# Optimization experiments

Measured on AMD Instinct MI355X. Metric: run time of the kernel, lower is better.

Reference implementation:

```python
import jax, jax.numpy as jnp
import numpy as np

N_NODES, N_EDGES = 1600, 32000
C = 128            # sphere_channels
LMAX, MMAX = 6, 2
M0 = LMAX + 1      # number of m=0 coefficients (7)
N_SPH = (LMAX + 1) ** 2   # 49 full harmonics after inverse Wigner rotation
BASIS = 512        # distance expansion size
MAX_ELEM = 90
HID = 128
RESCALE = 23.395238876342773


def _build_to_m(lmax, mmax):
    # CoefficientMappingModule.to_m: permutation from l-primary to m-primary order
    m_c = []
    for l in range(lmax + 1):
        mm = min(mmax, l)
        m_c.extend(range(-mm, mm + 1))
    m_c = np.array(m_c)
    n = len(m_c)
    to_m = np.zeros((n, n), np.float32)
    off = 0
    for m in range(mmax + 1):
        idx_r = np.nonzero(m_c == m)[0]
        for o, i in enumerate(idx_r):
            to_m[o + off, i] = 1.0
        off += len(idx_r)
        if m > 0:
            idx_i = np.nonzero(m_c == -m)[0]
            for o, i in enumerate(idx_i):
                to_m[o + off, i] = 1.0
            off += len(idx_i)
    return to_m

_TO_M = _build_to_m(LMAX, MMAX)
N_ALL = _TO_M.shape[0]   # 29


def setup_inputs() -> dict:
    key = jax.random.key(0)
    ks = jax.random.split(key, 12)
    d_in = BASIS + 2 * HID   # 768 (distance basis + source/target atom embeddings)
    return {
        "atomic_numbers": jax.random.randint(ks[0], (N_NODES,), 0, MAX_ELEM),
        "edge_distance": jax.random.uniform(ks[1], (N_EDGES, BASIS), dtype=jnp.float32),
        "edge_index": jax.random.randint(ks[2], (2, N_EDGES), 0, N_NODES),
        "src_table": jax.random.uniform(ks[3], (MAX_ELEM, HID), minval=-0.001, maxval=0.001),
        "tgt_table": jax.random.uniform(ks[4], (MAX_ELEM, HID), minval=-0.001, maxval=0.001),
        "w1": jax.random.normal(ks[5], (d_in, HID)) / np.float32(np.sqrt(d_in)),
        "b1": jnp.zeros((HID,), jnp.float32),
        "g1": jnp.ones((HID,), jnp.float32),
        "be1": jnp.zeros((HID,), jnp.float32),
        "w2": jax.random.normal(ks[6], (HID, HID)) / np.float32(np.sqrt(HID)),
        "b2": jnp.zeros((HID,), jnp.float32),
        "g2": jnp.ones((HID,), jnp.float32),
        "be2": jnp.zeros((HID,), jnp.float32),
        "w3": jax.random.normal(ks[7], (HID, M0 * C)) / np.float32(np.sqrt(HID)),
        "b3": jnp.zeros((M0 * C,), jnp.float32),
        "to_m": jnp.asarray(_TO_M),
        "wigner_inv": jax.random.normal(ks[8], (N_EDGES, N_SPH, N_ALL)) * 0.2,
    }


def _ln(x, g, b, eps=1e-5):
    mu = jnp.mean(x, axis=-1, keepdims=True)
    var = jnp.var(x, axis=-1, keepdims=True)
    return (x - mu) * jax.lax.rsqrt(var + eps) * g + b


def reference(atomic_numbers, edge_distance, edge_index, src_table, tgt_table,
              w1, b1, g1, be1, w2, b2, g2, be2, w3, b3, to_m, wigner_inv):
    E = edge_distance.shape[0]
    # atom-edge embedding gathers
    src = src_table[atomic_numbers[edge_index[0]]]            # [E, HID]
    tgt = tgt_table[atomic_numbers[edge_index[1]]]            # [E, HID]
    x = jnp.concatenate([edge_distance, src, tgt], axis=1)    # [E, 768]
    # RadialFunction: Linear -> LN -> SiLU -> Linear -> LN -> SiLU -> Linear
    h = jax.nn.silu(_ln(x @ w1 + b1, g1, be1))
    h = jax.nn.silu(_ln(h @ w2 + b2, g2, be2))
    x0 = (h @ w3 + b3).reshape(E, M0, C)                      # m=0 coefficients
    # _l_primary: to_m.T @ emb. Padded rows (m != 0) are zero, so only the
    # first M0 rows of to_m contribute.
    x_l = jnp.einsum("emc,ml->elc", x0, to_m[:M0])            # [E, N_ALL, C]
    # _rotate_inv: per-edge inverse Wigner-D rotation to full harmonics
    x_rot = jnp.einsum("eij,ejc->eic", wigner_inv, x_l)       # [E, N_SPH, C]
    # _reduce_edge: scatter-add onto target nodes, then rescale
    out = jax.ops.segment_sum(x_rot, edge_index[1], num_segments=N_NODES)
    return out / RESCALE
```

## Files before the change

### kernel.cpp

```cpp
#include <hip/hip_runtime.h>
#include <hip/hip_bf16.h>

#define NE 32000
#define NNODES 1600
#define CCH 128
#define M0C 7
#define NSPH 49
#define NALLC 29
#define BASIS 512
#define DIN 768
#define HID 128
#define RESCALE_F 23.395238876342773f
#define CH 28
#define MAXCH (NE / CH + NNODES)

typedef __bf16 bf16x8 __attribute__((ext_vector_type(8)));
typedef __bf16 bf16x2 __attribute__((ext_vector_type(2)));
typedef float  f32x4  __attribute__((ext_vector_type(4)));

__device__ __forceinline__ float bf16_to_f(unsigned short v) {
    unsigned int u = ((unsigned int)v) << 16;
    return __uint_as_float(u);
}
__device__ __forceinline__ unsigned short f_to_bf16(float f) {
    unsigned int u = __float_as_uint(f);
    unsigned int r = (u + 0x7FFFu + ((u >> 16) & 1u)) >> 16;
    return (unsigned short)r;
}
__device__ __forceinline__ float silu_f(float x) {
    return x / (1.0f + __expf(-x));
}

__device__ __forceinline__ float dot2_bf16(unsigned int a, unsigned int b, float c) {
#if __has_builtin(__builtin_amdgcn_fdot2_f32_bf16)
    union { unsigned int u; bf16x2 h; } ua, ub;
    ua.u = a; ub.u = b;
    return __builtin_amdgcn_fdot2_f32_bf16(ua.h, ub.h, c, false);
#else
    float r = c;
    r = fmaf(__uint_as_float(a << 16), __uint_as_float(b << 16), r);
    r = fmaf(__uint_as_float(a & 0xFFFF0000u), __uint_as_float(b & 0xFFFF0000u), r);
    return r;
#endif
}

__global__ __launch_bounds__(256) void prepack_w(
    const float* __restrict__ w1, const float* __restrict__ w2, const float* __restrict__ w3,
    unsigned short* __restrict__ w1t,
    unsigned short* __restrict__ w2t,
    unsigned short* __restrict__ w3t)
{
    int idx = blockIdx.x * 256 + threadIdx.x;
    if (idx < 98304) {
        int n = idx / 768, k = idx - n * 768;
        w1t[idx] = f_to_bf16(w1[(size_t)k * 128 + n]);
    } else if (idx < 114688) {
        int j = idx - 98304;
        int n = j / 128, k = j - n * 128;
        w2t[j] = f_to_bf16(w2[(size_t)k * 128 + n]);
    } else if (idx < 229376) {
        int j = idx - 114688;
        int n = j / 128, k = j - n * 128;
        w3t[j] = f_to_bf16(w3[(size_t)k * 896 + n]);
    }
}

__global__ __launch_bounds__(256) void gemm1_ln_mfma(
    const float* __restrict__ dist,
    const int* __restrict__ edge_index,
    const int* __restrict__ atomic_numbers,
    const float* __restrict__ src_table,
    const float* __restrict__ tgt_table,
    const unsigned short* __restrict__ w1t,
    const float* __restrict__ bias,
    const float* __restrict__ gam,
    const float* __restrict__ bet,
    unsigned short* __restrict__ Out)
{
    const int t = threadIdx.x;
    const int wv = t >> 6, lane = t & 63;
    const int m = lane & 15, quad = lane >> 4;
    const int row0 = blockIdx.x * 64 + wv * 16;
    const int row = row0 + m;

    const int sid  = atomic_numbers[edge_index[row]];
    const int tid2 = atomic_numbers[edge_index[NE + row]];
    const float* a0 = dist + (size_t)row * 512 + quad * 8;
    const float* a1 = src_table + sid * 128 + quad * 8;
    const float* a2 = tgt_table + tid2 * 128 + quad * 8;
    const unsigned short* bb = w1t + (size_t)m * 768 + quad * 8;

    f32x4 acc[8] = {};

#pragma unroll
    for (int k0 = 0; k0 < 768; k0 += 32) {
        const float* ap = (k0 < 512) ? (a0 + k0)
                        : (k0 < 640) ? (a1 + (k0 - 512))
                                     : (a2 + (k0 - 640));
        float4 va = *(const float4*)ap;
        float4 vb = *(const float4*)(ap + 4);
        bf16x8 af;
        af[0] = (__bf16)va.x; af[1] = (__bf16)va.y;
        af[2] = (__bf16)va.z; af[3] = (__bf16)va.w;
        af[4] = (__bf16)vb.x; af[5] = (__bf16)vb.y;
        af[6] = (__bf16)vb.z; af[7] = (__bf16)vb.w;
#pragma unroll
        for (int ct = 0; ct < 8; ++ct) {
            bf16x8 bfv = *(const bf16x8*)(bb + (size_t)ct * 16 * 768 + k0);
            acc[ct] = __builtin_amdgcn_mfma_f32_16x16x32_bf16(af, bfv, acc[ct], 0, 0, 0);
        }
    }

    float bbv[8], ggv[8], eev[8];
#pragma unroll
    for (int ct = 0; ct < 8; ++ct) {
        bbv[ct] = bias[ct * 16 + m];
        ggv[ct] = gam[ct * 16 + m];
        eev[ct] = bet[ct * 16 + m];
    }
#pragma unroll
    for (int reg = 0; reg < 4; ++reg) {
        float v[8];
        float s = 0.f, s2 = 0.f;
#pragma unroll
        for (int ct = 0; ct < 8; ++ct) {
            v[ct] = acc[ct][reg] + bbv[ct];
            s += v[ct]; s2 += v[ct] * v[ct];
        }
#pragma unroll
        for (int off = 1; off < 16; off <<= 1) {
            s  += __shfl_xor(s, off, 64);
            s2 += __shfl_xor(s2, off, 64);
        }
        float mean = s * (1.0f / 128.0f);
        float var  = s2 * (1.0f / 128.0f) - mean * mean;
        float rstd = rsqrtf(var + 1e-5f);
        int orow = row0 + 4 * quad + reg;
#pragma unroll
        for (int ct = 0; ct < 8; ++ct) {
            float o = silu_f((v[ct] - mean) * rstd * ggv[ct] + eev[ct]);
            Out[(size_t)orow * 128 + ct * 16 + m] = f_to_bf16(o);
        }
    }
}

__global__ __launch_bounds__(256) void gemm2_ln_mfma(
    const unsigned short* __restrict__ A,
    const unsigned short* __restrict__ Bt,
    const float* __restrict__ bias,
    const float* __restrict__ gam,
    const float* __restrict__ bet,
    unsigned short* __restrict__ Out)
{
    const int t = threadIdx.x;
    const int wv = t >> 6, lane = t & 63;
    const int m = lane & 15, quad = lane >> 4;
    const int row0 = blockIdx.x * 64 + wv * 16;

    f32x4 acc[8] = {};
    const unsigned short* arow = A + (size_t)(row0 + m) * 128 + quad * 8;
    const unsigned short* bb   = Bt + (size_t)m * 128 + quad * 8;

#pragma unroll
    for (int k0 = 0; k0 < 128; k0 += 32) {
        bf16x8 af = *(const bf16x8*)(arow + k0);
#pragma unroll
        for (int ct = 0; ct < 8; ++ct) {
            bf16x8 bfv = *(const bf16x8*)(bb + (size_t)ct * 16 * 128 + k0);
            acc[ct] = __builtin_amdgcn_mfma_f32_16x16x32_bf16(af, bfv, acc[ct], 0, 0, 0);
        }
    }

    float bbv[8], ggv[8], eev[8];
#pragma unroll
    for (int ct = 0; ct < 8; ++ct) {
        bbv[ct] = bias[ct * 16 + m];
        ggv[ct] = gam[ct * 16 + m];
        eev[ct] = bet[ct * 16 + m];
    }
#pragma unroll
    for (int reg = 0; reg < 4; ++reg) {
        float v[8];
        float s = 0.f, s2 = 0.f;
#pragma unroll
        for (int ct = 0; ct < 8; ++ct) {
            v[ct] = acc[ct][reg] + bbv[ct];
            s += v[ct]; s2 += v[ct] * v[ct];
        }
#pragma unroll
        for (int off = 1; off < 16; off <<= 1) {
            s  += __shfl_xor(s, off, 64);
            s2 += __shfl_xor(s2, off, 64);
        }
        float mean = s * (1.0f / 128.0f);
        float var  = s2 * (1.0f / 128.0f) - mean * mean;
        float rstd = rsqrtf(var + 1e-5f);
        int row = row0 + 4 * quad + reg;
#pragma unroll
        for (int ct = 0; ct < 8; ++ct) {
            float o = silu_f((v[ct] - mean) * rstd * ggv[ct] + eev[ct]);
            Out[(size_t)row * 128 + ct * 16 + m] = f_to_bf16(o);
        }
    }
}

__global__ __launch_bounds__(256) void gemm3_mfma(
    const unsigned short* __restrict__ A,
    const unsigned short* __restrict__ w3t,
    const float* __restrict__ b3,
    unsigned short* __restrict__ X0p)
{
    const int t = threadIdx.x;
    const int wv = t >> 6, lane = t & 63;
    const int m = lane & 15, quad = lane >> 4;
    const int row0 = blockIdx.x * 16;
    const int c0 = wv * 32;

    f32x4 acc[14] = {};
    const unsigned short* arow = A + (size_t)(row0 + m) * 128 + quad * 8;

#pragma unroll
    for (int k0 = 0; k0 < 128; k0 += 32) {
        bf16x8 af = *(const bf16x8*)(arow + k0);
#pragma unroll
        for (int o = 0; o < 7; ++o) {
#pragma unroll
            for (int ch2 = 0; ch2 < 2; ++ch2) {
                const unsigned short* bb =
                    w3t + (size_t)(o * 128 + c0 + ch2 * 16 + m) * 128 + quad * 8 + k0;
                bf16x8 bfv = *(const bf16x8*)bb;
                acc[o * 2 + ch2] =
                    __builtin_amdgcn_mfma_f32_16x16x32_bf16(af, bfv, acc[o * 2 + ch2], 0, 0, 0);
            }
        }
    }

    const float inv_res = 1.0f / RESCALE_F;
    float bv[14];
#pragma unroll
    for (int o = 0; o < 7; ++o)
#pragma unroll
        for (int ch2 = 0; ch2 < 2; ++ch2)
            bv[o * 2 + ch2] = b3[o * 128 + c0 + ch2 * 16 + m];

#pragma unroll
    for (int reg = 0; reg < 4; ++reg) {
        int row = row0 + 4 * quad + reg;
#pragma unroll
        for (int ch2 = 0; ch2 < 2; ++ch2) {
            int c = c0 + ch2 * 16 + m;
            union { unsigned short us[8]; uint4 q; } pk;
#pragma unroll
            for (int o = 0; o < 7; ++o)
                pk.us[o] = f_to_bf16((acc[o * 2 + ch2][reg] + bv[o * 2 + ch2]) * inv_res);
            pk.us[7] = 0;
            *(uint4*)(X0p + (size_t)row * 1024 + c * 8) = pk.q;
        }
    }
}

__global__ __launch_bounds__(256) void hist_kernel(
    const int* __restrict__ edge_index, int* __restrict__ cnt)
{
    int e = blockIdx.x * 256 + threadIdx.x;
    if (e < NE) atomicAdd(&cnt[edge_index[NE + e]], 1);
}

__global__ __launch_bounds__(256) void scan_kernel(
    const int* __restrict__ cnt, int* __restrict__ offs, int* __restrict__ cur)
{
    __shared__ int part[256];
    const int t = threadIdx.x;
    const int base = t * 7;
    int s = 0;
#pragma unroll
    for (int j = 0; j < 7; ++j) {
        int i = base + j;
        if (i < NNODES) s += cnt[i];
    }
    part[t] = s;
    __syncthreads();
    for (int off = 1; off < 256; off <<= 1) {
        int v = (t >= off) ? part[t - off] : 0;
        __syncthreads();
        part[t] += v;
        __syncthreads();
    }
    int run = (t > 0) ? part[t - 1] : 0;
#pragma unroll
    for (int j = 0; j < 7; ++j) {
        int i = base + j;
        if (i < NNODES) {
            offs[i] = run;
            cur[i] = run;
            run += cnt[i];
        }
    }
    if (t == 0) offs[NNODES] = part[255];
}

__global__ __launch_bounds__(256) void scatter_kernel(
    const int* __restrict__ edge_index, int* __restrict__ cur, int* __restrict__ order)
{
    int e = blockIdx.x * 256 + threadIdx.x;
    if (e < NE) {
        int tgt = edge_index[NE + e];
        int pos = atomicAdd(&cur[tgt], 1);
        order[pos] = e;
    }
}

__global__ __launch_bounds__(256) void build_chunks(
    const int* __restrict__ offs, int* __restrict__ chunk_cnt,
    int* __restrict__ ch_node, int* __restrict__ ch_beg, int* __restrict__ ch_lm)
{
    int n = blockIdx.x * 256 + threadIdx.x;
    if (n >= NNODES) return;
    int b = offs[n], k = offs[n + 1] - b;
    if (k == 0) return;
    int nc = (k + CH - 1) / CH;
    int base = atomicAdd(chunk_cnt, nc);
    for (int c = 0; c < nc; ++c) {
        ch_node[base + c] = n;
        ch_beg[base + c]  = b + CH * c;
        int l = min(CH, k - CH * c);
        ch_lm[base + c] = l | ((nc > 1) ? 0x10000 : 0);
    }
}

__global__ __launch_bounds__(256) void rotate_chunks(
    const unsigned short* __restrict__ X0p,
    const float* __restrict__ wig,
    const int* __restrict__ order,
    const int* __restrict__ chunk_cnt,
    const int* __restrict__ ch_node,
    const int* __restrict__ ch_beg,
    const int* __restrict__ ch_lm,
    float* __restrict__ out)
{
    __shared__ unsigned short Ws[CH][NSPH][8];
    __shared__ int es[CH];

    const int b = blockIdx.x;
    if (b >= chunk_cnt[0]) return;
    const int node = ch_node[b];
    const int beg  = ch_beg[b];
    const int lm   = ch_lm[b];
    const int len  = lm & 0xFFFF;
    const int multi = lm >> 16;

    const int t = threadIdx.x;
    if (t < CH) es[t] = (t < len) ? order[beg + t] : 0;

    const int slot8 = t >> 3;
    const int lane8 = t & 7;
    if (slot8 < len) {
        const int e = order[beg + slot8];
        const float* wsrc = wig + (size_t)e * (NSPH * NALLC);
#pragma unroll
        for (int j = 0; j < 49; ++j) {
            int idx = j * 8 + lane8;
            int i = idx >> 3, o = idx & 7;
            float v = 0.f;
            if (o < 7) {
                int col = (o < 2) ? (2 * o) : (5 * o - 4);
                v = wsrc[i * NALLC + col];
            }
            Ws[slot8][i][o] = f_to_bf16(v);
        }
    }
    __syncthreads();

    const int cg = t & 31;
    const int rg = t >> 5;
    float acc[7][4];
#pragma unroll
    for (int r = 0; r < 7; ++r)
#pragma unroll
        for (int j = 0; j < 4; ++j) acc[r][j] = 0.0f;

    uint4 xq0, xq1, xq2, xq3;
    {
        const uint4* xp = (const uint4*)(X0p + (size_t)es[0] * 1024 + 32 * cg);
        xq0 = xp[0]; xq1 = xp[1]; xq2 = xp[2]; xq3 = xp[3];
    }
    for (int s = 0; s < len; ++s) {
        int snx = (s + 1 < len) ? (s + 1) : s;
        const uint4* xp = (const uint4*)(X0p + (size_t)es[snx] * 1024 + 32 * cg);
        uint4 xn0 = xp[0], xn1 = xp[1], xn2 = xp[2], xn3 = xp[3];

#pragma unroll
        for (int r = 0; r < 7; ++r) {
            int row = rg + 8 * r;
            if (row < NSPH) {
                uint4 wq = *(const uint4*)&Ws[s][row][0];
                float a0 = acc[r][0], a1 = acc[r][1], a2 = acc[r][2], a3 = acc[r][3];
                a0 = dot2_bf16(xq0.x, wq.x, a0);
                a0 = dot2_bf16(xq0.y, wq.y, a0);
                a0 = dot2_bf16(xq0.z, wq.z, a0);
                a0 = dot2_bf16(xq0.w, wq.w, a0);
                a1 = dot2_bf16(xq1.x, wq.x, a1);
                a1 = dot2_bf16(xq1.y, wq.y, a1);
                a1 = dot2_bf16(xq1.z, wq.z, a1);
                a1 = dot2_bf16(xq1.w, wq.w, a1);
                a2 = dot2_bf16(xq2.x, wq.x, a2);
                a2 = dot2_bf16(xq2.y, wq.y, a2);
                a2 = dot2_bf16(xq2.z, wq.z, a2);
                a2 = dot2_bf16(xq2.w, wq.w, a2);
                a3 = dot2_bf16(xq3.x, wq.x, a3);
                a3 = dot2_bf16(xq3.y, wq.y, a3);
                a3 = dot2_bf16(xq3.z, wq.z, a3);
                a3 = dot2_bf16(xq3.w, wq.w, a3);
                acc[r][0] = a0; acc[r][1] = a1; acc[r][2] = a2; acc[r][3] = a3;
            }
        }
        xq0 = xn0; xq1 = xn1; xq2 = xn2; xq3 = xn3;
    }

    float* op = out + (size_t)node * (NSPH * CCH);
    if (multi) {
#pragma unroll
        for (int r = 0; r < 7; ++r) {
            int row = rg + 8 * r;
            if (row < NSPH) {
#pragma unroll
                for (int j = 0; j < 4; ++j)
                    atomicAdd(&op[row * CCH + 4 * cg + j], acc[r][j]);
            }
        }
    } else {
#pragma unroll
        for (int r = 0; r < 7; ++r) {
            int row = rg + 8 * r;
            if (row < NSPH) {
                *(float4*)&op[row * CCH + 4 * cg] =
                    make_float4(acc[r][0], acc[r][1], acc[r][2], acc[r][3]);
            }
        }
    }
}

extern "C" void kernel_launch(void* const* d_in, const int* in_sizes, int n_in,
                              void* d_out, int out_size, void* d_ws, size_t ws_size,
                              hipStream_t stream) {
    const int*   atomic_numbers = (const int*)d_in[0];
    const float* edge_distance  = (const float*)d_in[1];
    const int*   edge_index     = (const int*)d_in[2];
    const float* src_table      = (const float*)d_in[3];
    const float* tgt_table      = (const float*)d_in[4];
    const float* w1  = (const float*)d_in[5];
    const float* b1  = (const float*)d_in[6];
    const float* g1  = (const float*)d_in[7];
    const float* be1 = (const float*)d_in[8];
    const float* w2  = (const float*)d_in[9];
    const float* b2  = (const float*)d_in[10];
    const float* g2  = (const float*)d_in[11];
    const float* be2 = (const float*)d_in[12];
    const float* w3  = (const float*)d_in[13];
    const float* b3  = (const float*)d_in[14];
    const float* wig = (const float*)d_in[16];

    char* ws = (char*)d_ws;
    unsigned short* H1b = (unsigned short*)(ws);
    unsigned short* H2b = (unsigned short*)(ws + 8192000);
    unsigned short* X0p = (unsigned short*)(ws + 16384000);
    unsigned short* w1t = (unsigned short*)(ws + 81920000);
    unsigned short* w2t = (unsigned short*)(ws + 82116608);
    unsigned short* w3t = (unsigned short*)(ws + 82149376);
    int* ints      = (int*)(ws + 82378752);
    int* cnt       = ints;
    int* chunk_cnt = cnt + NNODES;
    int* offs      = chunk_cnt + 1;
    int* cur       = offs + NNODES + 1;
    int* order     = cur + NNODES;
    int* ch_node   = order + NE;
    int* ch_beg    = ch_node + MAXCH;
    int* ch_lm     = ch_beg + MAXCH;

    hipMemsetAsync(cnt, 0, (NNODES + 1) * sizeof(int), stream);
    hipMemsetAsync(d_out, 0, (size_t)out_size * sizeof(float), stream);

    hist_kernel<<<(NE + 255) / 256, 256, 0, stream>>>(edge_index, cnt);
    scan_kernel<<<1, 256, 0, stream>>>(cnt, offs, cur);
    scatter_kernel<<<(NE + 255) / 256, 256, 0, stream>>>(edge_index, cur, order);
    build_chunks<<<(NNODES + 255) / 256, 256, 0, stream>>>(
        offs, chunk_cnt, ch_node, ch_beg, ch_lm);

    prepack_w<<<(229376 + 255) / 256, 256, 0, stream>>>(w1, w2, w3, w1t, w2t, w3t);
    gemm1_ln_mfma<<<NE / 64, 256, 0, stream>>>(
        edge_distance, edge_index, atomic_numbers, src_table, tgt_table,
        w1t, b1, g1, be1, H1b);
    gemm2_ln_mfma<<<NE / 64, 256, 0, stream>>>(H1b, w2t, b2, g2, be2, H2b);
    gemm3_mfma<<<NE / 16, 256, 0, stream>>>(H2b, w3t, b3, X0p);

    rotate_chunks<<<MAXCH, 256, 0, stream>>>(
        X0p, wig, order, chunk_cnt, ch_node, ch_beg, ch_lm, (float*)d_out);
}
```

Before: 541.6 us.

## Pre-swizzle weights into MFMA fragment order and use one block per node

Weights are now packed so each lane's B-fragment for an MFMA step is contiguous, which gives fully coalesced 16-byte loads in all three GEMMs. The rotate stage drops the chunk table and atomics: each block owns one node and loops over its edges in chunks of 28, so the output memset and the build_chunks kernel go away. Wigner rows are loaded coalesced (whole 49x29 rows per wave, then filtered) instead of as strided column gathers. The trade-off is that high-degree nodes are serialised inside one block, giving less parallelism and possible load imbalance.

```diff
diff --git a/kernel.cpp b/kernel.cpp
--- a/kernel.cpp
+++ b/kernel.cpp
@@ -12,16 +12,11 @@
 #define HID 128
 #define RESCALE_F 23.395238876342773f
 #define CH 28
-#define MAXCH (NE / CH + NNODES)
 
 typedef __bf16 bf16x8 __attribute__((ext_vector_type(8)));
 typedef __bf16 bf16x2 __attribute__((ext_vector_type(2)));
 typedef float  f32x4  __attribute__((ext_vector_type(4)));
 
-__device__ __forceinline__ float bf16_to_f(unsigned short v) {
-    unsigned int u = ((unsigned int)v) << 16;
-    return __uint_as_float(u);
-}
 __device__ __forceinline__ unsigned short f_to_bf16(float f) {
     unsigned int u = __float_as_uint(f);
     unsigned int r = (u + 0x7FFFu + ((u >> 16) & 1u)) >> 16;
@@ -46,22 +41,42 @@
 
 __global__ __launch_bounds__(256) void prepack_w(
     const float* __restrict__ w1, const float* __restrict__ w2, const float* __restrict__ w3,
-    unsigned short* __restrict__ w1t,
-    unsigned short* __restrict__ w2t,
-    unsigned short* __restrict__ w3t)
+    unsigned short* __restrict__ w1p,
+    unsigned short* __restrict__ w2p,
+    unsigned short* __restrict__ w3p)
 {
     int idx = blockIdx.x * 256 + threadIdx.x;
     if (idx < 98304) {
-        int n = idx / 768, k = idx - n * 768;
-        w1t[idx] = f_to_bf16(w1[(size_t)k * 128 + n]);
+        int kstep = idx >> 12;
+        int ct    = (idx >> 9) & 7;
+        int li    = idx & 511;
+        int lane = li >> 3, j = li & 7;
+        int m = lane & 15, quad = lane >> 4;
+        int k = kstep * 32 + quad * 8 + j;
+        int n = ct * 16 + m;
+        w1p[idx] = f_to_bf16(w1[(size_t)k * 128 + n]);
     } else if (idx < 114688) {
-        int j = idx - 98304;
-        int n = j / 128, k = j - n * 128;
-        w2t[j] = f_to_bf16(w2[(size_t)k * 128 + n]);
+        int j2 = idx - 98304;
+        int kstep = j2 >> 12;
+        int ct    = (j2 >> 9) & 7;
+        int li    = j2 & 511;
+        int lane = li >> 3, j = li & 7;
+        int m = lane & 15, quad = lane >> 4;
+        int k = kstep * 32 + quad * 8 + j;
+        int n = ct * 16 + m;
+        w2p[j2] = f_to_bf16(w2[(size_t)k * 128 + n]);
     } else if (idx < 229376) {
-        int j = idx - 114688;
-        int n = j / 128, k = j - n * 128;
-        w3t[j] = f_to_bf16(w3[(size_t)k * 896 + n]);
+        int j3 = idx - 114688;
+        int kstep = j3 / 28672;
+        int r     = j3 - kstep * 28672;
+        int o     = r >> 12;
+        int ctile = (r >> 9) & 7;
+        int li    = r & 511;
+        int lane = li >> 3, j = li & 7;
+        int m = lane & 15, quad = lane >> 4;
+        int k = kstep * 32 + quad * 8 + j;
+        int n = o * 128 + ctile * 16 + m;
+        w3p[j3] = f_to_bf16(w3[(size_t)k * 896 + n]);
     }
 }
 
@@ -71,7 +86,7 @@
     const int* __restrict__ atomic_numbers,
     const float* __restrict__ src_table,
     const float* __restrict__ tgt_table,
-    const unsigned short* __restrict__ w1t,
+    const unsigned short* __restrict__ w1p,
     const float* __restrict__ bias,
     const float* __restrict__ gam,
     const float* __restrict__ bet,
@@ -88,7 +103,7 @@
     const float* a0 = dist + (size_t)row * 512 + quad * 8;
     const float* a1 = src_table + sid * 128 + quad * 8;
     const float* a2 = tgt_table + tid2 * 128 + quad * 8;
-    const unsigned short* bb = w1t + (size_t)m * 768 + quad * 8;
+    const unsigned short* bb = w1p + lane * 8;
 
     f32x4 acc[8] = {};
 
@@ -106,7 +121,7 @@
         af[6] = (__bf16)vb.z; af[7] = (__bf16)vb.w;
 #pragma unroll
         for (int ct = 0; ct < 8; ++ct) {
-            bf16x8 bfv = *(const bf16x8*)(bb + (size_t)ct * 16 * 768 + k0);
+            bf16x8 bfv = *(const bf16x8*)(bb + (size_t)(((k0 >> 5) * 8 + ct)) * 512);
             acc[ct] = __builtin_amdgcn_mfma_f32_16x16x32_bf16(af, bfv, acc[ct], 0, 0, 0);
         }
     }
@@ -146,7 +161,7 @@
 
 __global__ __launch_bounds__(256) void gemm2_ln_mfma(
     const unsigned short* __restrict__ A,
-    const unsigned short* __restrict__ Bt,
+    const unsigned short* __restrict__ w2p,
     const float* __restrict__ bias,
     const float* __restrict__ gam,
     const float* __restrict__ bet,
@@ -159,14 +174,14 @@
 
     f32x4 acc[8] = {};
     const unsigned short* arow = A + (size_t)(row0 + m) * 128 + quad * 8;
-    const unsigned short* bb   = Bt + (size_t)m * 128 + quad * 8;
+    const unsigned short* bb   = w2p + lane * 8;
 
 #pragma unroll
     for (int k0 = 0; k0 < 128; k0 += 32) {
         bf16x8 af = *(const bf16x8*)(arow + k0);
 #pragma unroll
         for (int ct = 0; ct < 8; ++ct) {
-            bf16x8 bfv = *(const bf16x8*)(bb + (size_t)ct * 16 * 128 + k0);
+            bf16x8 bfv = *(const bf16x8*)(bb + (size_t)(((k0 >> 5) * 8 + ct)) * 512);
             acc[ct] = __builtin_amdgcn_mfma_f32_16x16x32_bf16(af, bfv, acc[ct], 0, 0, 0);
         }
     }
@@ -206,7 +221,7 @@
 
 __global__ __launch_bounds__(256) void gemm3_mfma(
     const unsigned short* __restrict__ A,
-    const unsigned short* __restrict__ w3t,
+    const unsigned short* __restrict__ w3p,
     const float* __restrict__ b3,
     unsigned short* __restrict__ X0p)
 {
@@ -218,6 +233,7 @@
 
     f32x4 acc[14] = {};
     const unsigned short* arow = A + (size_t)(row0 + m) * 128 + quad * 8;
+    const unsigned short* bb   = w3p + lane * 8;
 
 #pragma unroll
     for (int k0 = 0; k0 < 128; k0 += 32) {
@@ -226,9 +242,8 @@
         for (int o = 0; o < 7; ++o) {
 #pragma unroll
             for (int ch2 = 0; ch2 < 2; ++ch2) {
-                const unsigned short* bb =
-                    w3t + (size_t)(o * 128 + c0 + ch2 * 16 + m) * 128 + quad * 8 + k0;
-                bf16x8 bfv = *(const bf16x8*)bb;
+                bf16x8 bfv = *(const bf16x8*)(bb +
+                    (size_t)((((k0 >> 5) * 7 + o) * 8 + (wv * 2 + ch2))) * 512);
                 acc[o * 2 + ch2] =
                     __builtin_amdgcn_mfma_f32_16x16x32_bf16(af, bfv, acc[o * 2 + ch2], 0, 0, 0);
             }
@@ -310,132 +325,105 @@
     }
 }
 
-__global__ __launch_bounds__(256) void build_chunks(
-    const int* __restrict__ offs, int* __restrict__ chunk_cnt,
-    int* __restrict__ ch_node, int* __restrict__ ch_beg, int* __restrict__ ch_lm)
-{
-    int n = blockIdx.x * 256 + threadIdx.x;
-    if (n >= NNODES) return;
-    int b = offs[n], k = offs[n + 1] - b;
-    if (k == 0) return;
-    int nc = (k + CH - 1) / CH;
-    int base = atomicAdd(chunk_cnt, nc);
-    for (int c = 0; c < nc; ++c) {
-        ch_node[base + c] = n;
-        ch_beg[base + c]  = b + CH * c;
-        int l = min(CH, k - CH * c);
-        ch_lm[base + c] = l | ((nc > 1) ? 0x10000 : 0);
-    }
-}
-
-__global__ __launch_bounds__(256) void rotate_chunks(
+__global__ __launch_bounds__(256) void rotate_nodes(
     const unsigned short* __restrict__ X0p,
     const float* __restrict__ wig,
     const int* __restrict__ order,
-    const int* __restrict__ chunk_cnt,
-    const int* __restrict__ ch_node,
-    const int* __restrict__ ch_beg,
-    const int* __restrict__ ch_lm,
+    const int* __restrict__ offs,
     float* __restrict__ out)
 {
     __shared__ unsigned short Ws[CH][NSPH][8];
     __shared__ int es[CH];
 
-    const int b = blockIdx.x;
-    if (b >= chunk_cnt[0]) return;
-    const int node = ch_node[b];
-    const int beg  = ch_beg[b];
-    const int lm   = ch_lm[b];
-    const int len  = lm & 0xFFFF;
-    const int multi = lm >> 16;
+    const int node = blockIdx.x;
+    const int beg = offs[node], end = offs[node + 1];
 
     const int t = threadIdx.x;
-    if (t < CH) es[t] = (t < len) ? order[beg + t] : 0;
-
-    const int slot8 = t >> 3;
-    const int lane8 = t & 7;
-    if (slot8 < len) {
-        const int e = order[beg + slot8];
-        const float* wsrc = wig + (size_t)e * (NSPH * NALLC);
-#pragma unroll
-        for (int j = 0; j < 49; ++j) {
-            int idx = j * 8 + lane8;
-            int i = idx >> 3, o = idx & 7;
-            float v = 0.f;
-            if (o < 7) {
-                int col = (o < 2) ? (2 * o) : (5 * o - 4);
-                v = wsrc[i * NALLC + col];
-            }
-            Ws[slot8][i][o] = f_to_bf16(v);
-        }
-    }
-    __syncthreads();
-
+    const int wv = t >> 6, lane = t & 63;
     const int cg = t & 31;
     const int rg = t >> 5;
+
     float acc[7][4];
 #pragma unroll
     for (int r = 0; r < 7; ++r)
 #pragma unroll
         for (int j = 0; j < 4; ++j) acc[r][j] = 0.0f;
 
-    uint4 xq0, xq1, xq2, xq3;
-    {
-        const uint4* xp = (const uint4*)(X0p + (size_t)es[0] * 1024 + 32 * cg);
-        xq0 = xp[0]; xq1 = xp[1]; xq2 = xp[2]; xq3 = xp[3];
-    }
-    for (int s = 0; s < len; ++s) {
-        int snx = (s + 1 < len) ? (s + 1) : s;
-        const uint4* xp = (const uint4*)(X0p + (size_t)es[snx] * 1024 + 32 * cg);
-        uint4 xn0 = xp[0], xn1 = xp[1], xn2 = xp[2], xn3 = xp[3];
-
-#pragma unroll
-        for (int r = 0; r < 7; ++r) {
-            int row = rg + 8 * r;
-            if (row < NSPH) {
-                uint4 wq = *(const uint4*)&Ws[s][row][0];
-                float a0 = acc[r][0], a1 = acc[r][1], a2 = acc[r][2], a3 = acc[r][3];
-                a0 = dot2_bf16(xq0.x, wq.x, a0);
-                a0 = dot2_bf16(xq0.y, wq.y, a0);
-                a0 = dot2_bf16(xq0.z, wq.z, a0);
-                a0 = dot2_bf16(xq0.w, wq.w, a0);
-                a1 = dot2_bf16(xq1.x, wq.x, a1);
-                a1 = dot2_bf16(xq1.y, wq.y, a1);
-                a1 = dot2_bf16(xq1.z, wq.z, a1);
-                a1 = dot2_bf16(xq1.w, wq.w, a1);
-                a2 = dot2_bf16(xq2.x, wq.x, a2);
-                a2 = dot2_bf16(xq2.y, wq.y, a2);
-                a2 = dot2_bf16(xq2.z, wq.z, a2);
-                a2 = dot2_bf16(xq2.w, wq.w, a2);
-                a3 = dot2_bf16(xq3.x, wq.x, a3);
-                a3 = dot2_bf16(xq3.y, wq.y, a3);
-                a3 = dot2_bf16(xq3.z, wq.z, a3);
-                a3 = dot2_bf16(xq3.w, wq.w, a3);
-                acc[r][0] = a0; acc[r][1] = a1; acc[r][2] = a2; acc[r][3] = a3;
+    for (int base = beg; base < end; base += CH) {
+        const int cnt = min(CH, end - base);
+        __syncthreads();
+        if (t < CH) es[t] = order[base + ((t < cnt) ? t : 0)];
+
+        for (int s = wv; s < cnt; s += 4) {
+            const int e = order[base + s];
+            const float* wsrc = wig + (size_t)e * (NSPH * NALLC);
+            if (lane < NSPH) Ws[s][lane][7] = 0;
+#pragma unroll
+            for (int it = 0; it < 23; ++it) {
+                int idx = it * 64 + lane;
+                if (idx < NSPH * NALLC) {
+                    float v = wsrc[idx];
+                    int i = idx / 29;
+                    int c = idx - i * 29;
+                    int o = -1;
+                    if (c == 0) o = 0;
+                    else if (c == 2) o = 1;
+                    else if (c >= 6) {
+                        int d = c - 6, q = d / 5;
+                        if (d - q * 5 == 0) o = q + 2;
+                    }
+                    if (o >= 0) Ws[s][i][o] = f_to_bf16(v);
+                }
             }
         }
-        xq0 = xn0; xq1 = xn1; xq2 = xn2; xq3 = xn3;
+        __syncthreads();
+
+        uint4 xq0, xq1, xq2, xq3;
+        {
+            const uint4* xp = (const uint4*)(X0p + (size_t)es[0] * 1024 + 32 * cg);
+            xq0 = xp[0]; xq1 = xp[1]; xq2 = xp[2]; xq3 = xp[3];
+        }
+        for (int s = 0; s < cnt; ++s) {
+            int snx = (s + 1 < cnt) ? (s + 1) : s;
+            const uint4* xp = (const uint4*)(X0p + (size_t)es[snx] * 1024 + 32 * cg);
+            uint4 xn0 = xp[0], xn1 = xp[1], xn2 = xp[2], xn3 = xp[3];
+
+#pragma unroll
+            for (int r = 0; r < 7; ++r) {
+                int row = rg + 8 * r;
+                if (row < NSPH) {
+                    uint4 wq = *(const uint4*)&Ws[s][row][0];
+                    float a0 = acc[r][0], a1 = acc[r][1], a2 = acc[r][2], a3 = acc[r][3];
+                    a0 = dot2_bf16(xq0.x, wq.x, a0);
+                    a0 = dot2_bf16(xq0.y, wq.y, a0);
+                    a0 = dot2_bf16(xq0.z, wq.z, a0);
+                    a0 = dot2_bf16(xq0.w, wq.w, a0);
+                    a1 = dot2_bf16(xq1.x, wq.x, a1);
+                    a1 = dot2_bf16(xq1.y, wq.y, a1);
+                    a1 = dot2_bf16(xq1.z, wq.z, a1);
+                    a1 = dot2_bf16(xq1.w, wq.w, a1);
+                    a2 = dot2_bf16(xq2.x, wq.x, a2);
+                    a2 = dot2_bf16(xq2.y, wq.y, a2);
+                    a2 = dot2_bf16(xq2.z, wq.z, a2);
+                    a2 = dot2_bf16(xq2.w, wq.w, a2);
+                    a3 = dot2_bf16(xq3.x, wq.x, a3);
+                    a3 = dot2_bf16(xq3.y, wq.y, a3);
+                    a3 = dot2_bf16(xq3.z, wq.z, a3);
+                    a3 = dot2_bf16(xq3.w, wq.w, a3);
+                    acc[r][0] = a0; acc[r][1] = a1; acc[r][2] = a2; acc[r][3] = a3;
+                }
+            }
+            xq0 = xn0; xq1 = xn1; xq2 = xn2; xq3 = xn3;
+        }
     }
 
     float* op = out + (size_t)node * (NSPH * CCH);
-    if (multi) {
-#pragma unroll
-        for (int r = 0; r < 7; ++r) {
-            int row = rg + 8 * r;
-            if (row < NSPH) {
-#pragma unroll
-                for (int j = 0; j < 4; ++j)
-                    atomicAdd(&op[row * CCH + 4 * cg + j], acc[r][j]);
-            }
-        }
-    } else {
-#pragma unroll
-        for (int r = 0; r < 7; ++r) {
-            int row = rg + 8 * r;
-            if (row < NSPH) {
-                *(float4*)&op[row * CCH + 4 * cg] =
-                    make_float4(acc[r][0], acc[r][1], acc[r][2], acc[r][3]);
-            }
+#pragma unroll
+    for (int r = 0; r < 7; ++r) {
+        int row = rg + 8 * r;
+        if (row < NSPH) {
+            *(float4*)&op[row * CCH + 4 * cg] =
+                make_float4(acc[r][0], acc[r][1], acc[r][2], acc[r][3]);
         }
     }
 }
@@ -464,35 +452,27 @@
     unsigned short* H1b = (unsigned short*)(ws);
     unsigned short* H2b = (unsigned short*)(ws + 8192000);
     unsigned short* X0p = (unsigned short*)(ws + 16384000);
-    unsigned short* w1t = (unsigned short*)(ws + 81920000);
-    unsigned short* w2t = (unsigned short*)(ws + 82116608);
-    unsigned short* w3t = (unsigned short*)(ws + 82149376);
+    unsigned short* w1p = (unsigned short*)(ws + 81920000);
+    unsigned short* w2p = (unsigned short*)(ws + 82116608);
+    unsigned short* w3p = (unsigned short*)(ws + 82149376);
     int* ints      = (int*)(ws + 82378752);
     int* cnt       = ints;
-    int* chunk_cnt = cnt + NNODES;
-    int* offs      = chunk_cnt + 1;
+    int* offs      = cnt + NNODES;
     int* cur       = offs + NNODES + 1;
     int* order     = cur + NNODES;
-    int* ch_node   = order + NE;
-    int* ch_beg    = ch_node + MAXCH;
-    int* ch_lm     = ch_beg + MAXCH;
-
-    hipMemsetAsync(cnt, 0, (NNODES + 1) * sizeof(int), stream);
-    hipMemsetAsync(d_out, 0, (size_t)out_size * sizeof(float), stream);
+
+    hipMemsetAsync(cnt, 0, NNODES * sizeof(int), stream);
 
     hist_kernel<<<(NE + 255) / 256, 256, 0, stream>>>(edge_index, cnt);
     scan_kernel<<<1, 256, 0, stream>>>(cnt, offs, cur);
     scatter_kernel<<<(NE + 255) / 256, 256, 0, stream>>>(edge_index, cur, order);
-    build_chunks<<<(NNODES + 255) / 256, 256, 0, stream>>>(
-        offs, chunk_cnt, ch_node, ch_beg, ch_lm);
-
-    prepack_w<<<(229376 + 255) / 256, 256, 0, stream>>>(w1, w2, w3, w1t, w2t, w3t);
+
+    prepack_w<<<(229376 + 255) / 256, 256, 0, stream>>>(w1, w2, w3, w1p, w2p, w3p);
     gemm1_ln_mfma<<<NE / 64, 256, 0, stream>>>(
         edge_distance, edge_index, atomic_numbers, src_table, tgt_table,
-        w1t, b1, g1, be1, H1b);
-    gemm2_ln_mfma<<<NE / 64, 256, 0, stream>>>(H1b, w2t, b2, g2, be2, H2b);
-    gemm3_mfma<<<NE / 16, 256, 0, stream>>>(H2b, w3t, b3, X0p);
-
-    rotate_chunks<<<MAXCH, 256, 0, stream>>>(
-        X0p, wig, order, chunk_cnt, ch_node, ch_beg, ch_lm, (float*)d_out);
-}
+        w1p, b1, g1, be1, H1b);
+    gemm2_ln_mfma<<<NE / 64, 256, 0, stream>>>(H1b, w2p, b2, g2, be2, H2b);
+    gemm3_mfma<<<NE / 16, 256, 0, stream>>>(H2b, w3p, b3, X0p);
+
+    rotate_nodes<<<NNODES, 256, 0, stream>>>(X0p, wig, order, offs, (float*)d_out);
+}
```

Result: slower. 645.4 us (+19.2%).
